# Optimization experiments

Measured on AMD Instinct MI355X. Metric: run time of the kernel, lower is better.

## Reference

```python
import jax, jax.numpy as jnp
import numpy as np

B, L, C = 8, 4096, 256  # batches, points per batch, channels
C8 = C // 8             # query/key projection dim


def setup_inputs() -> dict:
    key = jax.random.key(0)
    ks = jax.random.split(key, 8)
    feats = jax.random.normal(ks[0], (B * L, C), dtype=jnp.float32)
    s_in = 1.0 / np.sqrt(C)
    Wq = jax.random.normal(ks[1], (C8, C), dtype=jnp.float32) * s_in
    bq = jax.random.normal(ks[2], (C8,), dtype=jnp.float32) * 0.01
    Wk = jax.random.normal(ks[3], (C8, C), dtype=jnp.float32) * s_in
    bk = jax.random.normal(ks[4], (C8,), dtype=jnp.float32) * 0.01
    Wv = jax.random.normal(ks[5], (C, C), dtype=jnp.float32) * s_in
    bv = jax.random.normal(ks[6], (C,), dtype=jnp.float32) * 0.01
    # torch init is gamma=0 which zeroes the attention branch; use a nonzero
    # scalar so the attention path contributes to output/gradients.
    gamma = jnp.float32(0.5)
    return {"feats": feats, "Wq": Wq, "bq": bq, "Wk": Wk, "bk": bk,
            "Wv": Wv, "bv": bv, "gamma": gamma,
            "batch_size": B, "points_per_batch": L}


def reference(feats, Wq, bq, Wk, bk, Wv, bv, gamma, batch_size, points_per_batch):
    n, c = feats.shape
    x = feats.reshape(batch_size, points_per_batch, c)  # [B, L, C]
    # conv1d with kernel_size=1 == per-point linear projection
    q = jnp.einsum('blc,dc->bld', x, Wq) + bq  # [B, L, C8]
    k = jnp.einsum('blc,dc->bld', x, Wk) + bk  # [B, L, C8]
    v = jnp.einsum('blc,dc->bld', x, Wv) + bv  # [B, L, C]
    energy = jnp.einsum('bid,bjd->bij', q, k)  # unscaled scores [B, L, L]
    attn = jax.nn.softmax(energy, axis=-1)
    # torch: out[c, l] = sum_j V[c, j] * attn[l, j]  -> [B, C, L]
    out_cl = jnp.einsum('bjc,blj->bcl', v, attn)
    # faithful to torch .view(batch_size, C): raw reshape of [C, L] -> [L, C]
    out = out_cl.reshape(batch_size, points_per_batch, c)
    y = gamma * out + x
    return y.reshape(n, c)
```

## Files before the change

### kernel.cpp

```cpp
#include <hip/hip_runtime.h>

#define LOG2E 1.44269504088896340736f

typedef __attribute__((ext_vector_type(4))) float  f32x4;
typedef __attribute__((ext_vector_type(8))) __bf16 bf16x8;
typedef __attribute__((ext_vector_type(4))) __bf16 bf16x4;

static __device__ __forceinline__ f32x4 mfma16(bf16x8 a, bf16x8 b, f32x4 c) {
  return __builtin_amdgcn_mfma_f32_16x16x32_bf16(a, b, c, 0, 0, 0);
}


__global__ void cvt_f32_to_bf16(const float* __restrict__ s, __bf16* __restrict__ d, int n4) {
  const int stride = gridDim.x * blockDim.x;
  for (int i = blockIdx.x * blockDim.x + threadIdx.x; i < n4; i += stride) {
    const float4 v = reinterpret_cast<const float4*>(s)[i];
    bf16x4 o = { (__bf16)v.x, (__bf16)v.y, (__bf16)v.z, (__bf16)v.w };
    reinterpret_cast<bf16x4*>(d)[i] = o;
  }
}

__global__ __launch_bounds__(256) void cvt_weights(
    const float* __restrict__ wq, const float* __restrict__ wk, const float* __restrict__ wv,
    __bf16* __restrict__ dq, __bf16* __restrict__ dk, __bf16* __restrict__ dv) {
  const int i = blockIdx.x * 256 + threadIdx.x;
  const float* s; __bf16* d; int off;
  if (i < 2048)      { s = wq; d = dq; off = i; }
  else if (i < 4096) { s = wk; d = dk; off = i - 2048; }
  else               { s = wv; d = dv; off = i - 4096; }
  const float4 v = reinterpret_cast<const float4*>(s)[off];
  bf16x4 o = { (__bf16)v.x, (__bf16)v.y, (__bf16)v.z, (__bf16)v.w };
  reinterpret_cast<bf16x4*>(d)[off] = o;
}

__global__ __launch_bounds__(256) void qk_proj(
    const __bf16* __restrict__ x, const __bf16* __restrict__ wq, const __bf16* __restrict__ wk,
    const float* __restrict__ bq, const float* __restrict__ bk,
    __bf16* __restrict__ Qh, __bf16* __restrict__ Ql,
    __bf16* __restrict__ Kh, __bf16* __restrict__ Kl)
{
  const int w = threadIdx.x >> 6, lane = threadIdx.x & 63;
  const int lo = lane & 15, hi = lane >> 4;
  const int m0 = blockIdx.x * 64 + w * 16;
  f32x4 acc[4] = {};
  for (int ks = 0; ks < 8; ++ks) {
    const bf16x8 a = *reinterpret_cast<const bf16x8*>(x + (size_t)(m0 + lo) * 256 + ks * 32 + hi * 8);
    #pragma unroll
    for (int nt = 0; nt < 4; ++nt) {
      const int d = nt * 16 + lo;
      const __bf16* wrow = (nt < 2) ? (wq + d * 256) : (wk + (d - 32) * 256);
      const bf16x8 bfr = *reinterpret_cast<const bf16x8*>(wrow + ks * 32 + hi * 8);
      acc[nt] = mfma16(a, bfr, acc[nt]);
    }
  }
  #pragma unroll
  for (int nt = 0; nt < 4; ++nt) {
    const int d = nt * 16 + lo;
    const float bias = (nt < 2) ? bq[d] : bk[d - 32];
    #pragma unroll
    for (int r = 0; r < 4; ++r) {
      const size_t row = m0 + hi * 4 + r;
      float v = acc[nt][r] + bias;
      if (nt < 2) v *= LOG2E;
      const __bf16 vh = (__bf16)v;
      const __bf16 vl = (__bf16)(v - (float)vh);
      if (nt < 2) { Qh[row * 32 + d] = vh;        Ql[row * 32 + d] = vl; }
      else        { Kh[row * 32 + (d - 32)] = vh; Kl[row * 32 + (d - 32)] = vl; }
    }
  }
}

__global__ __launch_bounds__(256) void v_proj(
    const __bf16* __restrict__ x, const __bf16* __restrict__ wv, const float* __restrict__ bv,
    __bf16* __restrict__ VT)
{
  const int w = threadIdx.x >> 6, lane = threadIdx.x & 63;
  const int lo = lane & 15, hi = lane >> 4;
  const int bn = blockIdx.x & 511, bc = blockIdx.x >> 9;
  const int n0 = bn * 64;
  const int c0 = bc * 64 + w * 16;
  f32x4 acc[4] = {};
  for (int ks = 0; ks < 8; ++ks) {
    const bf16x8 a = *reinterpret_cast<const bf16x8*>(wv + (size_t)(c0 + lo) * 256 + ks * 32 + hi * 8);
    #pragma unroll
    for (int nt = 0; nt < 4; ++nt) {
      const bf16x8 bfr = *reinterpret_cast<const bf16x8*>(x + (size_t)(n0 + nt * 16 + lo) * 256 + ks * 32 + hi * 8);
      acc[nt] = mfma16(a, bfr, acc[nt]);
    }
  }
  const int bb = n0 >> 12;
  #pragma unroll
  for (int nt = 0; nt < 4; ++nt) {
    const int nl = n0 + nt * 16 + lo;
    #pragma unroll
    for (int r = 0; r < 4; ++r) {
      const int c = c0 + hi * 4 + r;
      VT[(size_t)(bb * 256 + c) * 4096 + (nl & 4095)] = (__bf16)(acc[nt][r] + bv[c]);
    }
  }
}

__global__ __launch_bounds__(256, 2) void attn_kernel(
    const __bf16* __restrict__ Qhi, const __bf16* __restrict__ Qlo,
    const __bf16* __restrict__ Khi, const __bf16* __restrict__ Klo,
    const __bf16* __restrict__ VT,
    const float* __restrict__ feats, const float* __restrict__ gptr,
    float* __restrict__ out)
{
  __shared__ alignas(16) __bf16 vlds[2][256 * 64];
  __shared__ alignas(16) __bf16 pbuf[4][16 * 64];

  const int tid  = threadIdx.x;
  const int w    = tid >> 6, lane = tid & 63;
  const int lo   = lane & 15, hi = lane >> 4;
  const int b    = blockIdx.x & 7;
  const int qt   = blockIdx.x >> 3;
  const int qblk = qt * 64;
  const int qw   = qblk + w * 16;

  const size_t qrow = (size_t)(b * 4096 + qw + lo) * 32 + hi * 8;
  const bf16x8 qh = *reinterpret_cast<const bf16x8*>(Qhi + qrow);
  const bf16x8 ql = *reinterpret_cast<const bf16x8*>(Qlo + qrow);

  const size_t kbase = (size_t)(b * 4096 + lo) * 32 + hi * 8;

  const int lsw = (lane & 7) ^ (lane >> 3);
  const __bf16* vstage_src0 = VT + (size_t)(b * 256 + w * 64 + (lane >> 3)) * 4096 + lsw * 8;

  char* const pw_base = (char*)&pbuf[w][0];
  const int swz = (lo & 7) << 4;

  f32x4 o[16] = {};
  f32x4 lacc4 = {0.f, 0.f, 0.f, 0.f};

  #define STAGE_V(JB, BUF)                                                        \
    {                                                                             \
      _Pragma("unroll")                                                           \
      for (int g = 0; g < 8; ++g) {                                               \
        __builtin_amdgcn_global_load_lds(                                         \
            (const __attribute__((address_space(1))) void*)(vstage_src0 + (size_t)g * 8 * 4096 + (JB)), \
            (__attribute__((address_space(3))) void*)(&vlds[BUF][(w * 64 + g * 8) * 64 + lane * 8]), \
            16, 0, 0);                                                            \
      }                                                                           \
    }

  STAGE_V(0, 0);
  bf16x8 kh[4], kl[4];
  #pragma unroll
  for (int jt = 0; jt < 4; ++jt) {
    kh[jt] = *reinterpret_cast<const bf16x8*>(Khi + kbase + (size_t)(jt * 16) * 32);
    kl[jt] = *reinterpret_cast<const bf16x8*>(Klo + kbase + (size_t)(jt * 16) * 32);
  }
  asm volatile("s_waitcnt vmcnt(0)" ::: "memory");
  __builtin_amdgcn_s_barrier();

  #pragma unroll 2
  for (int t = 0; t < 64; ++t) {
    const int jb  = t * 64;
    const int jn  = (jb + 64) & 4095;
    const int cur = t & 1, nxt = cur ^ 1;

    f32x4 s[4];
    #pragma unroll
    for (int jt = 0; jt < 4; ++jt) {
      f32x4 acc = {0.f, 0.f, 0.f, 0.f};
      acc = mfma16(kh[jt], qh, acc);
      acc = mfma16(kl[jt], qh, acc);
      acc = mfma16(kh[jt], ql, acc);
      s[jt] = acc;
    }

    STAGE_V(jn, nxt);
    asm volatile("" ::: "memory");
    __builtin_amdgcn_sched_barrier(0);

    bf16x8 kh2[4], kl2[4];
    #pragma unroll
    for (int jt = 0; jt < 4; ++jt) {
      kh2[jt] = *reinterpret_cast<const bf16x8*>(Khi + kbase + (size_t)(jn + jt * 16) * 32);
      kl2[jt] = *reinterpret_cast<const bf16x8*>(Klo + kbase + (size_t)(jn + jt * 16) * 32);
    }

    #pragma unroll
    for (int jt = 0; jt < 4; ++jt) {
      f32x4 p4;
      #pragma unroll
      for (int r = 0; r < 4; ++r) p4[r] = __builtin_amdgcn_exp2f(s[jt][r]);
      lacc4 += p4;
      bf16x4 pk = { (__bf16)p4[0], (__bf16)p4[1], (__bf16)p4[2], (__bf16)p4[3] };
      *reinterpret_cast<bf16x4*>(pw_base + lo * 128 + ((jt * 32 + hi * 8) ^ swz)) = pk;
    }

    bf16x8 pf[2];
    #pragma unroll
    for (int cc = 0; cc < 2; ++cc)
      pf[cc] = *reinterpret_cast<const bf16x8*>(pw_base + lo * 128 + ((cc * 64 + hi * 16) ^ swz));

    const __bf16* const vb_base = &vlds[cur][0];
    __builtin_amdgcn_s_setprio(1);
    #pragma unroll
    for (int cc = 0; cc < 2; ++cc) {
      #pragma unroll
      for (int ct = 0; ct < 16; ++ct) {
        const int c = ct * 16 + lo;
        const bf16x8 vb = *reinterpret_cast<const bf16x8*>(
            vb_base + c * 64 + ((((cc * 4 + hi) ^ (c & 7))) << 3));
        o[ct] = mfma16(pf[cc], vb, o[ct]);
      }
    }
    __builtin_amdgcn_s_setprio(0);

    asm volatile("s_waitcnt vmcnt(8) lgkmcnt(0)" ::: "memory");
    __builtin_amdgcn_sched_barrier(0);
    __builtin_amdgcn_s_barrier();
    asm volatile("" ::: "memory");
    __builtin_amdgcn_sched_barrier(0);

    #pragma unroll
    for (int jt = 0; jt < 4; ++jt) { kh[jt] = kh2[jt]; kl[jt] = kl2[jt]; }
  }
  #undef STAGE_V

  float lacc = lacc4[0] + lacc4[1] + lacc4[2] + lacc4[3];
  lacc += __shfl_xor(lacc, 16);
  lacc += __shfl_xor(lacc, 32);
  const float g = gptr[0];
  float inv[4];
  #pragma unroll
  for (int r = 0; r < 4; ++r) inv[r] = g / __shfl(lacc, hi * 4 + r);

  const size_t obase = (size_t)b * (256 * 4096);
  const int q_lo = qw + hi * 4;
  #pragma unroll
  for (int ct = 0; ct < 16; ++ct) {
    const int c = ct * 16 + lo;
    const size_t idx = obase + (size_t)c * 4096 + q_lo;
    const float4 xr = *reinterpret_cast<const float4*>(feats + idx);
    float4 y;
    y.x = o[ct][0] * inv[0] + xr.x;
    y.y = o[ct][1] * inv[1] + xr.y;
    y.z = o[ct][2] * inv[2] + xr.z;
    y.w = o[ct][3] * inv[3] + xr.w;
    *reinterpret_cast<float4*>(out + idx) = y;
  }
}

extern "C" void kernel_launch(void* const* d_in, const int* in_sizes, int n_in,
                              void* d_out, int out_size, void* d_ws, size_t ws_size,
                              hipStream_t stream) {
  const float* feats = (const float*)d_in[0];
  const float* Wq    = (const float*)d_in[1];
  const float* bq    = (const float*)d_in[2];
  const float* Wk    = (const float*)d_in[3];
  const float* bk    = (const float*)d_in[4];
  const float* Wv    = (const float*)d_in[5];
  const float* bv    = (const float*)d_in[6];
  const float* gamma = (const float*)d_in[7];
  float* out = (float*)d_out;

  char* ws = (char*)d_ws;
  const size_t SZ_X  = 16777216;
  const size_t SZ_QK = 2097152;
  const size_t SZ_VT = 16777216;
  const size_t NEED = SZ_X + 4 * SZ_QK + SZ_VT + 2 * 16384 + 131072;
  if (ws_size < NEED) return;

  __bf16* xb  = (__bf16*)(ws);
  __bf16* Qh  = (__bf16*)(ws + SZ_X);
  __bf16* Ql  = (__bf16*)(ws + SZ_X + SZ_QK);
  __bf16* Kh  = (__bf16*)(ws + SZ_X + 2 * SZ_QK);
  __bf16* Kl  = (__bf16*)(ws + SZ_X + 3 * SZ_QK);
  __bf16* VT  = (__bf16*)(ws + SZ_X + 4 * SZ_QK);
  __bf16* wqb = (__bf16*)(ws + SZ_X + 4 * SZ_QK + SZ_VT);
  __bf16* wkb = wqb + 32 * 256;
  __bf16* wvb = wkb + 32 * 256;

  cvt_f32_to_bf16<<<2048, 256, 0, stream>>>(feats, xb, 8388608 / 4);
  cvt_weights<<<80, 256, 0, stream>>>(Wq, Wk, Wv, wqb, wkb, wvb);

  qk_proj<<<512, 256, 0, stream>>>(xb, wqb, wkb, bq, bk, Qh, Ql, Kh, Kl);
  v_proj <<<2048, 256, 0, stream>>>(xb, wvb, bv, VT);
  attn_kernel<<<512, 256, 0, stream>>>(Qh, Ql, Kh, Kl, VT, feats, gamma, out);
}
```

Before: 190.5 us.

## Split attention key range across waves with 32x32 MFMA and LDS reduction

The attention kernel now gives each block 32 queries instead of 64 and splits each 64-key tile across the four waves. Each wave computes scores for its 16 keys, reads V fragments straight from global memory rather than staging them in LDS, and accumulates with 32x32x16 MFMAs. Partial outputs and row sums are then reduced across waves through LDS in a rotating exchange, and the grid doubles to 1024 blocks. The v_proj store is also changed to write packed bf16x4 vectors. This removes the per-iteration V staging and barrier, in exchange for more global V traffic (no reuse across waves) and a reduction epilogue that needs a large shared buffer.

```diff
diff --git a/kernel.cpp b/kernel.cpp
--- a/kernel.cpp
+++ b/kernel.cpp
@@ -2,12 +2,16 @@
 
 #define LOG2E 1.44269504088896340736f
 
-typedef __attribute__((ext_vector_type(4))) float  f32x4;
-typedef __attribute__((ext_vector_type(8))) __bf16 bf16x8;
-typedef __attribute__((ext_vector_type(4))) __bf16 bf16x4;
+typedef __attribute__((ext_vector_type(4)))  float  f32x4;
+typedef __attribute__((ext_vector_type(16))) float  f32x16;
+typedef __attribute__((ext_vector_type(8)))  __bf16 bf16x8;
+typedef __attribute__((ext_vector_type(4)))  __bf16 bf16x4;
 
 static __device__ __forceinline__ f32x4 mfma16(bf16x8 a, bf16x8 b, f32x4 c) {
   return __builtin_amdgcn_mfma_f32_16x16x32_bf16(a, b, c, 0, 0, 0);
+}
+static __device__ __forceinline__ f32x16 mfma32(bf16x8 a, bf16x8 b, f32x16 c) {
+  return __builtin_amdgcn_mfma_f32_32x32x16_bf16(a, b, c, 0, 0, 0);
 }
 
 
@@ -85,18 +89,18 @@
     #pragma unroll
     for (int nt = 0; nt < 4; ++nt) {
       const bf16x8 bfr = *reinterpret_cast<const bf16x8*>(x + (size_t)(n0 + nt * 16 + lo) * 256 + ks * 32 + hi * 8);
-      acc[nt] = mfma16(a, bfr, acc[nt]);
+      acc[nt] = mfma16(bfr, a, acc[nt]);
     }
   }
   const int bb = n0 >> 12;
+  const int c = c0 + lo;
+  const float bias = bv[c];
   #pragma unroll
   for (int nt = 0; nt < 4; ++nt) {
-    const int nl = n0 + nt * 16 + lo;
-    #pragma unroll
-    for (int r = 0; r < 4; ++r) {
-      const int c = c0 + hi * 4 + r;
-      VT[(size_t)(bb * 256 + c) * 4096 + (nl & 4095)] = (__bf16)(acc[nt][r] + bv[c]);
-    }
+    const int n = (n0 + nt * 16 + hi * 4) & 4095;
+    bf16x4 pk = { (__bf16)(acc[nt][0] + bias), (__bf16)(acc[nt][1] + bias),
+                  (__bf16)(acc[nt][2] + bias), (__bf16)(acc[nt][3] + bias) };
+    *reinterpret_cast<bf16x4*>(VT + (size_t)(bb * 256 + c) * 4096 + n) = pk;
   }
 }
 
@@ -107,142 +111,156 @@
     const float* __restrict__ feats, const float* __restrict__ gptr,
     float* __restrict__ out)
 {
-  __shared__ alignas(16) __bf16 vlds[2][256 * 64];
-  __shared__ alignas(16) __bf16 pbuf[4][16 * 64];
+  __shared__ alignas(16) __bf16 pt[4][32 * 24];
+  __shared__ alignas(16) float  ored[4][2048];
+  __shared__ float lred[4][32];
+  __shared__ float lsumbuf[32];
 
   const int tid  = threadIdx.x;
   const int w    = tid >> 6, lane = tid & 63;
   const int lo   = lane & 15, hi = lane >> 4;
+  const int l31  = lane & 31, h  = lane >> 5;
   const int b    = blockIdx.x & 7;
-  const int qt   = blockIdx.x >> 3;
-  const int qblk = qt * 64;
-  const int qw   = qblk + w * 16;
-
-  const size_t qrow = (size_t)(b * 4096 + qw + lo) * 32 + hi * 8;
-  const bf16x8 qh = *reinterpret_cast<const bf16x8*>(Qhi + qrow);
-  const bf16x8 ql = *reinterpret_cast<const bf16x8*>(Qlo + qrow);
-
-  const size_t kbase = (size_t)(b * 4096 + lo) * 32 + hi * 8;
-
-  const int lsw = (lane & 7) ^ (lane >> 3);
-  const __bf16* vstage_src0 = VT + (size_t)(b * 256 + w * 64 + (lane >> 3)) * 4096 + lsw * 8;
-
-  char* const pw_base = (char*)&pbuf[w][0];
-  const int swz = (lo & 7) << 4;
-
-  f32x4 o[16] = {};
-  f32x4 lacc4 = {0.f, 0.f, 0.f, 0.f};
-
-  #define STAGE_V(JB, BUF)                                                        \
-    {                                                                             \
-      _Pragma("unroll")                                                           \
-      for (int g = 0; g < 8; ++g) {                                               \
-        __builtin_amdgcn_global_load_lds(                                         \
-            (const __attribute__((address_space(1))) void*)(vstage_src0 + (size_t)g * 8 * 4096 + (JB)), \
-            (__attribute__((address_space(3))) void*)(&vlds[BUF][(w * 64 + g * 8) * 64 + lane * 8]), \
-            16, 0, 0);                                                            \
-      }                                                                           \
-    }
-
-  STAGE_V(0, 0);
-  bf16x8 kh[4], kl[4];
-  #pragma unroll
-  for (int jt = 0; jt < 4; ++jt) {
-    kh[jt] = *reinterpret_cast<const bf16x8*>(Khi + kbase + (size_t)(jt * 16) * 32);
-    kl[jt] = *reinterpret_cast<const bf16x8*>(Klo + kbase + (size_t)(jt * 16) * 32);
-  }
-  asm volatile("s_waitcnt vmcnt(0)" ::: "memory");
-  __builtin_amdgcn_s_barrier();
-
-  #pragma unroll 2
+  const int qb   = blockIdx.x >> 3;
+
+  bf16x8 qh[2], ql[2];
+  #pragma unroll
+  for (int qt = 0; qt < 2; ++qt) {
+    const int qi = (b * 4096 + qb * 32 + qt * 16 + lo) * 32 + hi * 8;
+    qh[qt] = *reinterpret_cast<const bf16x8*>(Qhi + qi);
+    ql[qt] = *reinterpret_cast<const bf16x8*>(Qlo + qi);
+  }
+
+  const int kidx = (b * 4096 + w * 16 + lo) * 32 + hi * 8;
+  int voff[8];
+  #pragma unroll
+  for (int ct = 0; ct < 8; ++ct)
+    voff[ct] = (b * 256 + ct * 32 + l31) * 4096 + w * 16 + h * 8;
+
+  char* const ptw = (char*)&pt[w][0];
+
+  f32x16 o[8] = {};
+  f32x4  lacc4[2] = {};
+
+  bf16x8 kh = *reinterpret_cast<const bf16x8*>(Khi + kidx);
+  bf16x8 kl = *reinterpret_cast<const bf16x8*>(Klo + kidx);
+
   for (int t = 0; t < 64; ++t) {
-    const int jb  = t * 64;
-    const int jn  = (jb + 64) & 4095;
-    const int cur = t & 1, nxt = cur ^ 1;
-
-    f32x4 s[4];
-    #pragma unroll
-    for (int jt = 0; jt < 4; ++jt) {
-      f32x4 acc = {0.f, 0.f, 0.f, 0.f};
-      acc = mfma16(kh[jt], qh, acc);
-      acc = mfma16(kl[jt], qh, acc);
-      acc = mfma16(kh[jt], ql, acc);
-      s[jt] = acc;
-    }
-
-    STAGE_V(jn, nxt);
-    asm volatile("" ::: "memory");
-    __builtin_amdgcn_sched_barrier(0);
-
-    bf16x8 kh2[4], kl2[4];
-    #pragma unroll
-    for (int jt = 0; jt < 4; ++jt) {
-      kh2[jt] = *reinterpret_cast<const bf16x8*>(Khi + kbase + (size_t)(jn + jt * 16) * 32);
-      kl2[jt] = *reinterpret_cast<const bf16x8*>(Klo + kbase + (size_t)(jn + jt * 16) * 32);
-    }
-
-    #pragma unroll
-    for (int jt = 0; jt < 4; ++jt) {
+    const int jb = t * 64;
+    const int jn = (jb + 64) & 4095;
+
+    bf16x8 vf[8];
+    #pragma unroll
+    for (int ct = 0; ct < 8; ++ct)
+      vf[ct] = *reinterpret_cast<const bf16x8*>(VT + voff[ct] + jb);
+
+    const bf16x8 kh2 = *reinterpret_cast<const bf16x8*>(Khi + kidx + jn * 32);
+    const bf16x8 kl2 = *reinterpret_cast<const bf16x8*>(Klo + kidx + jn * 32);
+
+    f32x4 s[2];
+    #pragma unroll
+    for (int qt = 0; qt < 2; ++qt) {
+      f32x4 a = {0.f, 0.f, 0.f, 0.f};
+      a = mfma16(kh, qh[qt], a);
+      a = mfma16(kl, qh[qt], a);
+      a = mfma16(kh, ql[qt], a);
+      s[qt] = a;
+    }
+
+    #pragma unroll
+    for (int qt = 0; qt < 2; ++qt) {
       f32x4 p4;
       #pragma unroll
-      for (int r = 0; r < 4; ++r) p4[r] = __builtin_amdgcn_exp2f(s[jt][r]);
-      lacc4 += p4;
+      for (int r = 0; r < 4; ++r) p4[r] = __builtin_amdgcn_exp2f(s[qt][r]);
+      lacc4[qt] += p4;
       bf16x4 pk = { (__bf16)p4[0], (__bf16)p4[1], (__bf16)p4[2], (__bf16)p4[3] };
-      *reinterpret_cast<bf16x4*>(pw_base + lo * 128 + ((jt * 32 + hi * 8) ^ swz)) = pk;
-    }
-
-    bf16x8 pf[2];
-    #pragma unroll
-    for (int cc = 0; cc < 2; ++cc)
-      pf[cc] = *reinterpret_cast<const bf16x8*>(pw_base + lo * 128 + ((cc * 64 + hi * 16) ^ swz));
-
-    const __bf16* const vb_base = &vlds[cur][0];
+      *reinterpret_cast<bf16x4*>(ptw + (qt * 16 + lo) * 48 + hi * 8) = pk;
+    }
+
+    const bf16x8 pa = *reinterpret_cast<const bf16x8*>(ptw + l31 * 48 + h * 16);
+
     __builtin_amdgcn_s_setprio(1);
     #pragma unroll
-    for (int cc = 0; cc < 2; ++cc) {
-      #pragma unroll
-      for (int ct = 0; ct < 16; ++ct) {
-        const int c = ct * 16 + lo;
-        const bf16x8 vb = *reinterpret_cast<const bf16x8*>(
-            vb_base + c * 64 + ((((cc * 4 + hi) ^ (c & 7))) << 3));
-        o[ct] = mfma16(pf[cc], vb, o[ct]);
-      }
-    }
+    for (int ct = 0; ct < 8; ++ct)
+      o[ct] = mfma32(pa, vf[ct], o[ct]);
     __builtin_amdgcn_s_setprio(0);
 
-    asm volatile("s_waitcnt vmcnt(8) lgkmcnt(0)" ::: "memory");
-    __builtin_amdgcn_sched_barrier(0);
-    __builtin_amdgcn_s_barrier();
-    asm volatile("" ::: "memory");
-    __builtin_amdgcn_sched_barrier(0);
-
-    #pragma unroll
-    for (int jt = 0; jt < 4; ++jt) { kh[jt] = kh2[jt]; kl[jt] = kl2[jt]; }
-  }
-  #undef STAGE_V
-
-  float lacc = lacc4[0] + lacc4[1] + lacc4[2] + lacc4[3];
-  lacc += __shfl_xor(lacc, 16);
-  lacc += __shfl_xor(lacc, 32);
+    kh = kh2; kl = kl2;
+  }
+
+  float la0 = lacc4[0][0] + lacc4[0][1] + lacc4[0][2] + lacc4[0][3];
+  float la1 = lacc4[1][0] + lacc4[1][1] + lacc4[1][2] + lacc4[1][3];
+  la0 += __shfl_xor(la0, 16); la0 += __shfl_xor(la0, 32);
+  la1 += __shfl_xor(la1, 16); la1 += __shfl_xor(la1, 32);
+  if (lane < 16) { lred[w][lane] = la0; lred[w][16 + lane] = la1; }
+  __syncthreads();
+  if (w == 0 && lane < 32)
+    lsumbuf[lane] = lred[0][lane] + lred[1][lane] + lred[2][lane] + lred[3][lane];
+  __syncthreads();
+
   const float g = gptr[0];
-  float inv[4];
-  #pragma unroll
-  for (int r = 0; r < 4; ++r) inv[r] = g / __shfl(lacc, hi * 4 + r);
-
-  const size_t obase = (size_t)b * (256 * 4096);
-  const int q_lo = qw + hi * 4;
-  #pragma unroll
-  for (int ct = 0; ct < 16; ++ct) {
-    const int c = ct * 16 + lo;
-    const size_t idx = obase + (size_t)c * 4096 + q_lo;
-    const float4 xr = *reinterpret_cast<const float4*>(feats + idx);
-    float4 y;
-    y.x = o[ct][0] * inv[0] + xr.x;
-    y.y = o[ct][1] * inv[1] + xr.y;
-    y.z = o[ct][2] * inv[2] + xr.z;
-    y.w = o[ct][3] * inv[3] + xr.w;
-    *reinterpret_cast<float4*>(out + idx) = y;
-  }
+  f32x4 inv4[4];
+  #pragma unroll
+  for (int k = 0; k < 4; ++k) {
+    const f32x4 lv = *reinterpret_cast<const f32x4*>(&lsumbuf[8 * k + 4 * h]);
+    inv4[k][0] = g / lv[0]; inv4[k][1] = g / lv[1];
+    inv4[k][2] = g / lv[2]; inv4[k][3] = g / lv[3];
+  }
+
+  #define OADDR(REG, CL, K) ((char*)&ored[REG][0] + (CL) * 128 + ((((2*(K)+h) ^ ((CL) & 7))) << 4))
+  #define SEND(M)                                                              \
+    { _Pragma("unroll") for (int ti = 0; ti < 2; ++ti) {                       \
+        const int cl = ti * 32 + l31;                                          \
+        _Pragma("unroll") for (int k = 0; k < 4; ++k) {                        \
+          f32x4 v = { o[2*(M)+ti][4*k], o[2*(M)+ti][4*k+1],                    \
+                      o[2*(M)+ti][4*k+2], o[2*(M)+ti][4*k+3] };                \
+          *reinterpret_cast<f32x4*>(OADDR(w, cl, k)) = v; } } }
+  #define RECV(M, SRC)                                                         \
+    { _Pragma("unroll") for (int ti = 0; ti < 2; ++ti) {                       \
+        const int cl = ti * 32 + l31;                                          \
+        _Pragma("unroll") for (int k = 0; k < 4; ++k) {                        \
+          const f32x4 v = *reinterpret_cast<const f32x4*>(OADDR(SRC, cl, k));  \
+          o[2*(M)+ti][4*k]   += v[0]; o[2*(M)+ti][4*k+1] += v[1];              \
+          o[2*(M)+ti][4*k+2] += v[2]; o[2*(M)+ti][4*k+3] += v[3]; } } }
+
+  #pragma unroll
+  for (int r = 1; r < 4; ++r) {
+    const int m = (w + r) & 3;
+    if      (m == 0) SEND(0)
+    else if (m == 1) SEND(1)
+    else if (m == 2) SEND(2)
+    else             SEND(3)
+    __syncthreads();
+    const int src = (w - r) & 3;
+    if      (w == 0) RECV(0, src)
+    else if (w == 1) RECV(1, src)
+    else if (w == 2) RECV(2, src)
+    else             RECV(3, src)
+    __syncthreads();
+  }
+  #undef OADDR
+  #undef SEND
+  #undef RECV
+
+  const int obase = b * (256 * 4096);
+  const int q0 = qb * 32 + 4 * h;
+  #define EPI(M)                                                               \
+    { _Pragma("unroll") for (int ti = 0; ti < 2; ++ti) {                       \
+        const int c = (2*(M)+ti) * 32 + l31;                                   \
+        _Pragma("unroll") for (int k = 0; k < 4; ++k) {                        \
+          const int idx = obase + c * 4096 + q0 + 8 * k;                       \
+          const float4 xr = *reinterpret_cast<const float4*>(feats + idx);     \
+          float4 y;                                                            \
+          y.x = o[2*(M)+ti][4*k]   * inv4[k][0] + xr.x;                        \
+          y.y = o[2*(M)+ti][4*k+1] * inv4[k][1] + xr.y;                        \
+          y.z = o[2*(M)+ti][4*k+2] * inv4[k][2] + xr.z;                        \
+          y.w = o[2*(M)+ti][4*k+3] * inv4[k][3] + xr.w;                        \
+          *reinterpret_cast<float4*>(out + idx) = y; } } }
+  if      (w == 0) EPI(0)
+  else if (w == 1) EPI(1)
+  else if (w == 2) EPI(2)
+  else             EPI(3)
+  #undef EPI
 }
 
 extern "C" void kernel_launch(void* const* d_in, const int* in_sizes, int n_in,
@@ -280,5 +298,5 @@
 
   qk_proj<<<512, 256, 0, stream>>>(xb, wqb, wkb, bq, bk, Qh, Ql, Kh, Kl);
   v_proj <<<2048, 256, 0, stream>>>(xb, wvb, bv, VT);
-  attn_kernel<<<512, 256, 0, stream>>>(Qh, Ql, Kh, Kl, VT, feats, gamma, out);
-}
+  attn_kernel<<<1024, 256, 0, stream>>>(Qh, Ql, Kh, Kl, VT, feats, gamma, out);
+}
```

After: 340.6 us. 78.8% more time.

## Switch PV product to 32x32x16 MFMA with 2x2 wave tiling

Applied to the files above, without the earlier changes.

Restructures the attention kernel so each wave owns 32 queries by 128 channels and computes P·V with 32x32x16 bf16 MFMAs instead of sixteen 16x16 tiles covering all 256 channels. This cuts the number of V LDS fragment reads per MFMA FLOP. V staging and the P buffer get new XOR swizzles, and row-sum normalization goes through LDS. The v_proj kernel also swaps MFMA operands so it writes packed bf16x4 vectors along the point dimension instead of scalar stores. The trade-off is that QK scores are now computed twice (each wave pair duplicates them for the same queries), and more layout complexity carries a risk of bank conflicts.

```diff
diff --git a/kernel.cpp b/kernel.cpp
--- a/kernel.cpp
+++ b/kernel.cpp
@@ -2,12 +2,16 @@
 
 #define LOG2E 1.44269504088896340736f
 
-typedef __attribute__((ext_vector_type(4))) float  f32x4;
-typedef __attribute__((ext_vector_type(8))) __bf16 bf16x8;
-typedef __attribute__((ext_vector_type(4))) __bf16 bf16x4;
+typedef __attribute__((ext_vector_type(4)))  float  f32x4;
+typedef __attribute__((ext_vector_type(16))) float  f32x16;
+typedef __attribute__((ext_vector_type(8)))  __bf16 bf16x8;
+typedef __attribute__((ext_vector_type(4)))  __bf16 bf16x4;
 
 static __device__ __forceinline__ f32x4 mfma16(bf16x8 a, bf16x8 b, f32x4 c) {
   return __builtin_amdgcn_mfma_f32_16x16x32_bf16(a, b, c, 0, 0, 0);
+}
+static __device__ __forceinline__ f32x16 mfma32(bf16x8 a, bf16x8 b, f32x16 c) {
+  return __builtin_amdgcn_mfma_f32_32x32x16_bf16(a, b, c, 0, 0, 0);
 }
 
 
@@ -85,18 +89,18 @@
     #pragma unroll
     for (int nt = 0; nt < 4; ++nt) {
       const bf16x8 bfr = *reinterpret_cast<const bf16x8*>(x + (size_t)(n0 + nt * 16 + lo) * 256 + ks * 32 + hi * 8);
-      acc[nt] = mfma16(a, bfr, acc[nt]);
+      acc[nt] = mfma16(bfr, a, acc[nt]);
     }
   }
   const int bb = n0 >> 12;
+  const int c = c0 + lo;
+  const float bias = bv[c];
   #pragma unroll
   for (int nt = 0; nt < 4; ++nt) {
-    const int nl = n0 + nt * 16 + lo;
-    #pragma unroll
-    for (int r = 0; r < 4; ++r) {
-      const int c = c0 + hi * 4 + r;
-      VT[(size_t)(bb * 256 + c) * 4096 + (nl & 4095)] = (__bf16)(acc[nt][r] + bv[c]);
-    }
+    const int n = (n0 + nt * 16 + hi * 4) & 4095;
+    bf16x4 pk = { (__bf16)(acc[nt][0] + bias), (__bf16)(acc[nt][1] + bias),
+                  (__bf16)(acc[nt][2] + bias), (__bf16)(acc[nt][3] + bias) };
+    *reinterpret_cast<bf16x4*>(VT + (size_t)(bb * 256 + c) * 4096 + n) = pk;
   }
 }
 
@@ -107,49 +111,69 @@
     const float* __restrict__ feats, const float* __restrict__ gptr,
     float* __restrict__ out)
 {
-  __shared__ alignas(16) __bf16 vlds[2][256 * 64];
-  __shared__ alignas(16) __bf16 pbuf[4][16 * 64];
+  __shared__ alignas(16) __bf16 vlds[2][16384];
+  __shared__ alignas(16) __bf16 pbuf[4][2048];
 
   const int tid  = threadIdx.x;
   const int w    = tid >> 6, lane = tid & 63;
   const int lo   = lane & 15, hi = lane >> 4;
+  const int l31  = lane & 31, h  = lane >> 5;
+  const int qg   = w & 1,    cg  = w >> 1;
   const int b    = blockIdx.x & 7;
-  const int qt   = blockIdx.x >> 3;
-  const int qblk = qt * 64;
-  const int qw   = qblk + w * 16;
-
-  const size_t qrow = (size_t)(b * 4096 + qw + lo) * 32 + hi * 8;
-  const bf16x8 qh = *reinterpret_cast<const bf16x8*>(Qhi + qrow);
-  const bf16x8 ql = *reinterpret_cast<const bf16x8*>(Qlo + qrow);
-
-  const size_t kbase = (size_t)(b * 4096 + lo) * 32 + hi * 8;
-
-  const int lsw = (lane & 7) ^ (lane >> 3);
-  const __bf16* vstage_src0 = VT + (size_t)(b * 256 + w * 64 + (lane >> 3)) * 4096 + lsw * 8;
-
-  char* const pw_base = (char*)&pbuf[w][0];
-  const int swz = (lo & 7) << 4;
-
-  f32x4 o[16] = {};
-  f32x4 lacc4 = {0.f, 0.f, 0.f, 0.f};
-
-  #define STAGE_V(JB, BUF)                                                        \
-    {                                                                             \
-      _Pragma("unroll")                                                           \
-      for (int g = 0; g < 8; ++g) {                                               \
-        __builtin_amdgcn_global_load_lds(                                         \
-            (const __attribute__((address_space(1))) void*)(vstage_src0 + (size_t)g * 8 * 4096 + (JB)), \
-            (__attribute__((address_space(3))) void*)(&vlds[BUF][(w * 64 + g * 8) * 64 + lane * 8]), \
-            16, 0, 0);                                                            \
-      }                                                                           \
+  const int qblk = (blockIdx.x >> 3) * 64;
+  const int qw   = qblk + qg * 32;
+
+  bf16x8 qh[2], ql[2];
+  #pragma unroll
+  for (int qt = 0; qt < 2; ++qt) {
+    const int qi = (b * 4096 + qw + qt * 16 + lo) * 32 + hi * 8;
+    qh[qt] = *reinterpret_cast<const bf16x8*>(Qhi + qi);
+    ql[qt] = *reinterpret_cast<const bf16x8*>(Qlo + qi);
+  }
+
+  const int kbase = (b * 4096 + lo) * 32 + hi * 8;
+
+  const int cc   = tid >> 3;
+  const int scc  = (tid & 7) ^ ((cc ^ (cc >> 3)) & 7);
+  const __bf16* const vsrc = VT + (size_t)(b * 256 + cc) * 4096;
+
+  int vrow[4], vsw[4];
+  #pragma unroll
+  for (int ct = 0; ct < 4; ++ct) {
+    const int row = cg * 128 + ct * 32 + l31;
+    vrow[ct] = row * 128;
+    vsw[ct]  = (row ^ (row >> 3)) & 7;
+  }
+  int swzq[2];
+  #pragma unroll
+  for (int qt = 0; qt < 2; ++qt) {
+    const int q = qt * 16 + lo;
+    swzq[qt] = (q ^ (q >> 3)) & 7;
+  }
+  const int swzp = (l31 ^ (l31 >> 3)) & 7;
+  char* const pwb = (char*)&pbuf[w][0];
+
+  f32x16 o[4] = {};
+  f32x4  lacc[2] = {};
+
+  #define STAGE_V(JB, BUF)                                                      \
+    {                                                                           \
+      _Pragma("unroll")                                                         \
+      for (int g = 0; g < 8; ++g) {                                             \
+        const int slot = scc ^ ((g & 1) << 2);                                  \
+        __builtin_amdgcn_global_load_lds(                                       \
+            (const __attribute__((address_space(1))) void*)(vsrc + (size_t)g * 32 * 4096 + (JB) + slot * 8), \
+            (__attribute__((address_space(3))) void*)(&vlds[BUF][g * 2048 + tid * 8]), \
+            16, 0, 0);                                                          \
+      }                                                                         \
     }
 
   STAGE_V(0, 0);
   bf16x8 kh[4], kl[4];
   #pragma unroll
   for (int jt = 0; jt < 4; ++jt) {
-    kh[jt] = *reinterpret_cast<const bf16x8*>(Khi + kbase + (size_t)(jt * 16) * 32);
-    kl[jt] = *reinterpret_cast<const bf16x8*>(Klo + kbase + (size_t)(jt * 16) * 32);
+    kh[jt] = *reinterpret_cast<const bf16x8*>(Khi + kbase + (jt * 16) * 32);
+    kl[jt] = *reinterpret_cast<const bf16x8*>(Klo + kbase + (jt * 16) * 32);
   }
   asm volatile("s_waitcnt vmcnt(0)" ::: "memory");
   __builtin_amdgcn_s_barrier();
@@ -160,14 +184,36 @@
     const int jn  = (jb + 64) & 4095;
     const int cur = t & 1, nxt = cur ^ 1;
 
-    f32x4 s[4];
-    #pragma unroll
-    for (int jt = 0; jt < 4; ++jt) {
-      f32x4 acc = {0.f, 0.f, 0.f, 0.f};
-      acc = mfma16(kh[jt], qh, acc);
-      acc = mfma16(kl[jt], qh, acc);
-      acc = mfma16(kh[jt], ql, acc);
-      s[jt] = acc;
+    #pragma unroll
+    for (int jp = 0; jp < 2; ++jp) {
+      f32x4 s[2][2];
+      #pragma unroll
+      for (int jj = 0; jj < 2; ++jj) {
+        const int jt = jp * 2 + jj;
+        #pragma unroll
+        for (int qt = 0; qt < 2; ++qt) {
+          f32x4 a = {0.f, 0.f, 0.f, 0.f};
+          a = mfma16(kh[jt], qh[qt], a);
+          a = mfma16(kl[jt], qh[qt], a);
+          a = mfma16(kh[jt], ql[qt], a);
+          s[jj][qt] = a;
+        }
+      }
+      #pragma unroll
+      for (int jj = 0; jj < 2; ++jj) {
+        const int jt = jp * 2 + jj;
+        #pragma unroll
+        for (int qt = 0; qt < 2; ++qt) {
+          f32x4 p4;
+          #pragma unroll
+          for (int r = 0; r < 4; ++r) p4[r] = __builtin_amdgcn_exp2f(s[jj][qt][r]);
+          lacc[qt] += p4;
+          bf16x4 pk = { (__bf16)p4[0], (__bf16)p4[1], (__bf16)p4[2], (__bf16)p4[3] };
+          const int q = qt * 16 + lo;
+          *reinterpret_cast<bf16x4*>(pwb + q * 128 +
+              (((jt * 2 + (hi >> 1)) ^ swzq[qt]) << 4) + ((hi & 1) << 3)) = pk;
+        }
+      }
     }
 
     STAGE_V(jn, nxt);
@@ -177,35 +223,24 @@
     bf16x8 kh2[4], kl2[4];
     #pragma unroll
     for (int jt = 0; jt < 4; ++jt) {
-      kh2[jt] = *reinterpret_cast<const bf16x8*>(Khi + kbase + (size_t)(jn + jt * 16) * 32);
-      kl2[jt] = *reinterpret_cast<const bf16x8*>(Klo + kbase + (size_t)(jn + jt * 16) * 32);
-    }
-
-    #pragma unroll
-    for (int jt = 0; jt < 4; ++jt) {
-      f32x4 p4;
+      kh2[jt] = *reinterpret_cast<const bf16x8*>(Khi + kbase + (jn + jt * 16) * 32);
+      kl2[jt] = *reinterpret_cast<const bf16x8*>(Klo + kbase + (jn + jt * 16) * 32);
+    }
+
+    bf16x8 pa[4];
+    #pragma unroll
+    for (int ks = 0; ks < 4; ++ks)
+      pa[ks] = *reinterpret_cast<const bf16x8*>(pwb + l31 * 128 + (((ks * 2 + h) ^ swzp) << 4));
+
+    const char* const vb = (const char*)&vlds[cur][0];
+    __builtin_amdgcn_s_setprio(1);
+    #pragma unroll
+    for (int ct = 0; ct < 4; ++ct) {
       #pragma unroll
-      for (int r = 0; r < 4; ++r) p4[r] = __builtin_amdgcn_exp2f(s[jt][r]);
-      lacc4 += p4;
-      bf16x4 pk = { (__bf16)p4[0], (__bf16)p4[1], (__bf16)p4[2], (__bf16)p4[3] };
-      *reinterpret_cast<bf16x4*>(pw_base + lo * 128 + ((jt * 32 + hi * 8) ^ swz)) = pk;
-    }
-
-    bf16x8 pf[2];
-    #pragma unroll
-    for (int cc = 0; cc < 2; ++cc)
-      pf[cc] = *reinterpret_cast<const bf16x8*>(pw_base + lo * 128 + ((cc * 64 + hi * 16) ^ swz));
-
-    const __bf16* const vb_base = &vlds[cur][0];
-    __builtin_amdgcn_s_setprio(1);
-    #pragma unroll
-    for (int cc = 0; cc < 2; ++cc) {
-      #pragma unroll
-      for (int ct = 0; ct < 16; ++ct) {
-        const int c = ct * 16 + lo;
-        const bf16x8 vb = *reinterpret_cast<const bf16x8*>(
-            vb_base + c * 64 + ((((cc * 4 + hi) ^ (c & 7))) << 3));
-        o[ct] = mfma16(pf[cc], vb, o[ct]);
+      for (int ks = 0; ks < 4; ++ks) {
+        const bf16x8 vf = *reinterpret_cast<const bf16x8*>(
+            vb + vrow[ct] + (((ks * 2 + h) ^ vsw[ct]) << 4));
+        o[ct] = mfma32(pa[ks], vf, o[ct]);
       }
     }
     __builtin_amdgcn_s_setprio(0);
@@ -221,27 +256,39 @@
   }
   #undef STAGE_V
 
-  float lacc = lacc4[0] + lacc4[1] + lacc4[2] + lacc4[3];
-  lacc += __shfl_xor(lacc, 16);
-  lacc += __shfl_xor(lacc, 32);
+  float la0 = lacc[0][0] + lacc[0][1] + lacc[0][2] + lacc[0][3];
+  float la1 = lacc[1][0] + lacc[1][1] + lacc[1][2] + lacc[1][3];
+  la0 += __shfl_xor(la0, 16); la0 += __shfl_xor(la0, 32);
+  la1 += __shfl_xor(la1, 16); la1 += __shfl_xor(la1, 32);
+  asm volatile("s_waitcnt lgkmcnt(0)" ::: "memory");
+  float* const lredw = (float*)&pbuf[w][0];
+  if (lane < 16) { lredw[lane] = la0; lredw[16 + lane] = la1; }
+
   const float g = gptr[0];
-  float inv[4];
-  #pragma unroll
-  for (int r = 0; r < 4; ++r) inv[r] = g / __shfl(lacc, hi * 4 + r);
-
-  const size_t obase = (size_t)b * (256 * 4096);
-  const int q_lo = qw + hi * 4;
-  #pragma unroll
-  for (int ct = 0; ct < 16; ++ct) {
-    const int c = ct * 16 + lo;
-    const size_t idx = obase + (size_t)c * 4096 + q_lo;
-    const float4 xr = *reinterpret_cast<const float4*>(feats + idx);
-    float4 y;
-    y.x = o[ct][0] * inv[0] + xr.x;
-    y.y = o[ct][1] * inv[1] + xr.y;
-    y.z = o[ct][2] * inv[2] + xr.z;
-    y.w = o[ct][3] * inv[3] + xr.w;
-    *reinterpret_cast<float4*>(out + idx) = y;
+  f32x4 inv[4];
+  #pragma unroll
+  for (int a = 0; a < 4; ++a) {
+    const f32x4 lv = *reinterpret_cast<const f32x4*>(&lredw[8 * a + 4 * h]);
+    inv[a][0] = g / lv[0]; inv[a][1] = g / lv[1];
+    inv[a][2] = g / lv[2]; inv[a][3] = g / lv[3];
+  }
+
+  const int obase = b * (256 * 4096);
+  const int q0 = qblk + qg * 32 + 4 * h;
+  #pragma unroll
+  for (int ct = 0; ct < 4; ++ct) {
+    const int c = cg * 128 + ct * 32 + l31;
+    #pragma unroll
+    for (int a = 0; a < 4; ++a) {
+      const int idx = obase + c * 4096 + q0 + 8 * a;
+      const float4 xr = *reinterpret_cast<const float4*>(feats + idx);
+      float4 y;
+      y.x = o[ct][4 * a]     * inv[a][0] + xr.x;
+      y.y = o[ct][4 * a + 1] * inv[a][1] + xr.y;
+      y.z = o[ct][4 * a + 2] * inv[a][2] + xr.z;
+      y.w = o[ct][4 * a + 3] * inv[a][3] + xr.w;
+      *reinterpret_cast<float4*>(out + idx) = y;
+    }
   }
 }
 
```

Measured after the change: 212.5 us. +11.6%, slower.

## Restructure attention to 8-wave blocks with 32x32 MFMA PV and software-pipelined P

Applied to the files above, without the earlier changes.

The attention kernel moves to 512-thread blocks. Work is split into 4 query tiles by 2 key halves for the score stage, and each wave owns 32 channels for the PV stage using 32x32x16 MFMAs on a shared P buffer. The P·V product for the previous tile is overlapped with loading and scoring the next tile through double-buffered P and V in LDS, and row sums are combined across waves through LDS at the end. The V projection is also changed to write packed bf16x4 transposed stores instead of scalar ones. The aims are better MFMA efficiency and fewer, wider stores, at the cost of more LDS traffic, a block-wide barrier every iteration and higher occupancy demands.

```diff
diff --git a/kernel.cpp b/kernel.cpp
--- a/kernel.cpp
+++ b/kernel.cpp
@@ -2,12 +2,16 @@
 
 #define LOG2E 1.44269504088896340736f
 
-typedef __attribute__((ext_vector_type(4))) float  f32x4;
-typedef __attribute__((ext_vector_type(8))) __bf16 bf16x8;
-typedef __attribute__((ext_vector_type(4))) __bf16 bf16x4;
+typedef __attribute__((ext_vector_type(4)))  float  f32x4;
+typedef __attribute__((ext_vector_type(16))) float  f32x16;
+typedef __attribute__((ext_vector_type(8)))  __bf16 bf16x8;
+typedef __attribute__((ext_vector_type(4)))  __bf16 bf16x4;
 
 static __device__ __forceinline__ f32x4 mfma16(bf16x8 a, bf16x8 b, f32x4 c) {
   return __builtin_amdgcn_mfma_f32_16x16x32_bf16(a, b, c, 0, 0, 0);
+}
+static __device__ __forceinline__ f32x16 mfma32(bf16x8 a, bf16x8 b, f32x16 c) {
+  return __builtin_amdgcn_mfma_f32_32x32x16_bf16(a, b, c, 0, 0, 0);
 }
 
 
@@ -85,163 +89,202 @@
     #pragma unroll
     for (int nt = 0; nt < 4; ++nt) {
       const bf16x8 bfr = *reinterpret_cast<const bf16x8*>(x + (size_t)(n0 + nt * 16 + lo) * 256 + ks * 32 + hi * 8);
-      acc[nt] = mfma16(a, bfr, acc[nt]);
+      acc[nt] = mfma16(bfr, a, acc[nt]);
     }
   }
   const int bb = n0 >> 12;
+  const int c = c0 + lo;
+  const float bias = bv[c];
   #pragma unroll
   for (int nt = 0; nt < 4; ++nt) {
-    const int nl = n0 + nt * 16 + lo;
-    #pragma unroll
-    for (int r = 0; r < 4; ++r) {
-      const int c = c0 + hi * 4 + r;
-      VT[(size_t)(bb * 256 + c) * 4096 + (nl & 4095)] = (__bf16)(acc[nt][r] + bv[c]);
-    }
-  }
-}
-
-__global__ __launch_bounds__(256, 2) void attn_kernel(
+    const int n = (n0 + nt * 16 + hi * 4) & 4095;
+    bf16x4 pk = { (__bf16)(acc[nt][0] + bias), (__bf16)(acc[nt][1] + bias),
+                  (__bf16)(acc[nt][2] + bias), (__bf16)(acc[nt][3] + bias) };
+    *reinterpret_cast<bf16x4*>(VT + (size_t)(bb * 256 + c) * 4096 + n) = pk;
+  }
+}
+
+__global__ __launch_bounds__(512, 4) void attn_kernel(
     const __bf16* __restrict__ Qhi, const __bf16* __restrict__ Qlo,
     const __bf16* __restrict__ Khi, const __bf16* __restrict__ Klo,
     const __bf16* __restrict__ VT,
     const float* __restrict__ feats, const float* __restrict__ gptr,
     float* __restrict__ out)
 {
-  __shared__ alignas(16) __bf16 vlds[2][256 * 64];
-  __shared__ alignas(16) __bf16 pbuf[4][16 * 64];
-
-  const int tid  = threadIdx.x;
-  const int w    = tid >> 6, lane = tid & 63;
-  const int lo   = lane & 15, hi = lane >> 4;
+  __shared__ alignas(16) __bf16 vlds[2][8][2048];
+  __shared__ alignas(16) __bf16 pbuf[2][4096];
+
+  const int tid = threadIdx.x;
+  const int w   = tid >> 6, lane = tid & 63;
+  const int lo  = lane & 15, hi = lane >> 4;
+  const int l31 = lane & 31, h  = lane >> 5;
+  const int qt  = w & 3, jtp = w >> 2;
   const int b    = blockIdx.x & 7;
-  const int qt   = blockIdx.x >> 3;
-  const int qblk = qt * 64;
-  const int qw   = qblk + w * 16;
-
-  const size_t qrow = (size_t)(b * 4096 + qw + lo) * 32 + hi * 8;
-  const bf16x8 qh = *reinterpret_cast<const bf16x8*>(Qhi + qrow);
-  const bf16x8 ql = *reinterpret_cast<const bf16x8*>(Qlo + qrow);
-
-  const size_t kbase = (size_t)(b * 4096 + lo) * 32 + hi * 8;
-
-  const int lsw = (lane & 7) ^ (lane >> 3);
-  const __bf16* vstage_src0 = VT + (size_t)(b * 256 + w * 64 + (lane >> 3)) * 4096 + lsw * 8;
-
-  char* const pw_base = (char*)&pbuf[w][0];
-  const int swz = (lo & 7) << 4;
-
-  f32x4 o[16] = {};
-  f32x4 lacc4 = {0.f, 0.f, 0.f, 0.f};
+  const int qblk = (blockIdx.x >> 3) * 64;
+
+  const int qi = (b * 4096 + qblk + qt * 16 + lo) * 32 + hi * 8;
+  const bf16x8 qh = *reinterpret_cast<const bf16x8*>(Qhi + qi);
+  const bf16x8 ql = *reinterpret_cast<const bf16x8*>(Qlo + qi);
+
+  const int kbase = (b * 4096 + jtp * 32 + lo) * 32 + hi * 8;
+
+  const int r_l = lane >> 3, s_l = lane & 7;
+  const __bf16* vsrc[4];
+  #pragma unroll
+  for (int g = 0; g < 4; ++g) {
+    const int row = w * 32 + g * 8 + r_l;
+    const int sw  = s_l ^ ((r_l ^ g) & 7);
+    vsrc[g] = VT + (size_t)(b * 256 + row) * 4096 + sw * 8;
+  }
+
+  const int q   = qt * 16 + lo;
+  const int swq = (q ^ (q >> 3)) & 7;
+  int swp[2], prow[2];
+  #pragma unroll
+  for (int qg = 0; qg < 2; ++qg) {
+    const int qq = qg * 32 + l31;
+    prow[qg] = qq * 128;
+    swp[qg]  = (qq ^ (qq >> 3)) & 7;
+  }
+  const int vrow = l31 * 128;
+  const int swv  = (l31 ^ (l31 >> 3)) & 7;
+
+  f32x16 o0 = {}, o1 = {};
+  f32x4  lacc = {};
 
   #define STAGE_V(JB, BUF)                                                        \
-    {                                                                             \
+    { _Pragma("unroll")                                                           \
+      for (int g = 0; g < 4; ++g) {                                               \
+        __builtin_amdgcn_global_load_lds(                                         \
+            (const __attribute__((address_space(1))) void*)(vsrc[g] + (JB)),      \
+            (__attribute__((address_space(3))) void*)(&vlds[BUF][w][g * 512 + lane * 8]), \
+            16, 0, 0);                                                            \
+      } }
+
+  #define PV_STEP(PRV)                                                            \
+    { const char* const pr = (const char*)&pbuf[PRV][0];                          \
+      const char* const vr = (const char*)&vlds[PRV][w][0] + vrow;                \
+      bf16x8 pa0[4], pa1[4], vf[4];                                               \
       _Pragma("unroll")                                                           \
-      for (int g = 0; g < 8; ++g) {                                               \
-        __builtin_amdgcn_global_load_lds(                                         \
-            (const __attribute__((address_space(1))) void*)(vstage_src0 + (size_t)g * 8 * 4096 + (JB)), \
-            (__attribute__((address_space(3))) void*)(&vlds[BUF][(w * 64 + g * 8) * 64 + lane * 8]), \
-            16, 0, 0);                                                            \
+      for (int ks = 0; ks < 4; ++ks) {                                            \
+        pa0[ks] = *reinterpret_cast<const bf16x8*>(pr + prow[0] + ((((ks * 2 + h) ^ swp[0])) << 4)); \
+        pa1[ks] = *reinterpret_cast<const bf16x8*>(pr + prow[1] + ((((ks * 2 + h) ^ swp[1])) << 4)); \
+        vf[ks]  = *reinterpret_cast<const bf16x8*>(vr + ((((ks * 2 + h) ^ swv)) << 4)); \
       }                                                                           \
-    }
-
-  STAGE_V(0, 0);
-  bf16x8 kh[4], kl[4];
-  #pragma unroll
-  for (int jt = 0; jt < 4; ++jt) {
-    kh[jt] = *reinterpret_cast<const bf16x8*>(Khi + kbase + (size_t)(jt * 16) * 32);
-    kl[jt] = *reinterpret_cast<const bf16x8*>(Klo + kbase + (size_t)(jt * 16) * 32);
-  }
-  asm volatile("s_waitcnt vmcnt(0)" ::: "memory");
-  __builtin_amdgcn_s_barrier();
-
-  #pragma unroll 2
-  for (int t = 0; t < 64; ++t) {
-    const int jb  = t * 64;
-    const int jn  = (jb + 64) & 4095;
-    const int cur = t & 1, nxt = cur ^ 1;
-
-    f32x4 s[4];
-    #pragma unroll
-    for (int jt = 0; jt < 4; ++jt) {
-      f32x4 acc = {0.f, 0.f, 0.f, 0.f};
-      acc = mfma16(kh[jt], qh, acc);
-      acc = mfma16(kl[jt], qh, acc);
-      acc = mfma16(kh[jt], ql, acc);
-      s[jt] = acc;
-    }
-
-    STAGE_V(jn, nxt);
-    asm volatile("" ::: "memory");
-    __builtin_amdgcn_sched_barrier(0);
-
-    bf16x8 kh2[4], kl2[4];
-    #pragma unroll
-    for (int jt = 0; jt < 4; ++jt) {
-      kh2[jt] = *reinterpret_cast<const bf16x8*>(Khi + kbase + (size_t)(jn + jt * 16) * 32);
-      kl2[jt] = *reinterpret_cast<const bf16x8*>(Klo + kbase + (size_t)(jn + jt * 16) * 32);
-    }
-
-    #pragma unroll
-    for (int jt = 0; jt < 4; ++jt) {
+      __builtin_amdgcn_s_setprio(1);                                              \
+      _Pragma("unroll")                                                           \
+      for (int ks = 0; ks < 4; ++ks) {                                            \
+        o0 = mfma32(pa0[ks], vf[ks], o0);                                         \
+        o1 = mfma32(pa1[ks], vf[ks], o1);                                         \
+      }                                                                           \
+      __builtin_amdgcn_s_setprio(0); }
+
+  {
+    const bf16x8 kh0 = *reinterpret_cast<const bf16x8*>(Khi + kbase);
+    const bf16x8 kl0 = *reinterpret_cast<const bf16x8*>(Klo + kbase);
+    const bf16x8 kh1 = *reinterpret_cast<const bf16x8*>(Khi + kbase + 512);
+    const bf16x8 kl1 = *reinterpret_cast<const bf16x8*>(Klo + kbase + 512);
+    STAGE_V(0, 0);
+    __builtin_amdgcn_sched_barrier(0);
+    #pragma unroll
+    for (int jj = 0; jj < 2; ++jj) {
+      const bf16x8 kh_ = jj ? kh1 : kh0;
+      const bf16x8 kl_ = jj ? kl1 : kl0;
+      f32x4 s_ = {0.f, 0.f, 0.f, 0.f};
+      s_ = mfma16(kh_, qh, s_);
+      s_ = mfma16(kl_, qh, s_);
+      s_ = mfma16(kh_, ql, s_);
       f32x4 p4;
       #pragma unroll
-      for (int r = 0; r < 4; ++r) p4[r] = __builtin_amdgcn_exp2f(s[jt][r]);
-      lacc4 += p4;
+      for (int r = 0; r < 4; ++r) p4[r] = __builtin_amdgcn_exp2f(s_[r]);
+      lacc += p4;
       bf16x4 pk = { (__bf16)p4[0], (__bf16)p4[1], (__bf16)p4[2], (__bf16)p4[3] };
-      *reinterpret_cast<bf16x4*>(pw_base + lo * 128 + ((jt * 32 + hi * 8) ^ swz)) = pk;
-    }
-
-    bf16x8 pf[2];
-    #pragma unroll
-    for (int cc = 0; cc < 2; ++cc)
-      pf[cc] = *reinterpret_cast<const bf16x8*>(pw_base + lo * 128 + ((cc * 64 + hi * 16) ^ swz));
-
-    const __bf16* const vb_base = &vlds[cur][0];
-    __builtin_amdgcn_s_setprio(1);
-    #pragma unroll
-    for (int cc = 0; cc < 2; ++cc) {
+      const int slot = ((jtp * 2 + jj) * 2 + (hi >> 1)) ^ swq;
+      *reinterpret_cast<bf16x4*>((char*)&pbuf[0][0] + q * 128 + (slot << 4) + ((hi & 1) << 3)) = pk;
+    }
+    asm volatile("s_waitcnt lgkmcnt(0)" ::: "memory");
+    __builtin_amdgcn_sched_barrier(0);
+    __builtin_amdgcn_s_barrier();
+  }
+
+  #pragma unroll 2
+  for (int t = 1; t < 64; ++t) {
+    const int jb  = t * 64;
+    const int cur = t & 1, prv = cur ^ 1;
+
+    asm volatile("s_waitcnt vmcnt(0)" ::: "memory");
+    __builtin_amdgcn_sched_barrier(0);
+
+    const bf16x8 kh0 = *reinterpret_cast<const bf16x8*>(Khi + kbase + jb * 32);
+    const bf16x8 kl0 = *reinterpret_cast<const bf16x8*>(Klo + kbase + jb * 32);
+    const bf16x8 kh1 = *reinterpret_cast<const bf16x8*>(Khi + kbase + jb * 32 + 512);
+    const bf16x8 kl1 = *reinterpret_cast<const bf16x8*>(Klo + kbase + jb * 32 + 512);
+    STAGE_V(jb, cur);
+    __builtin_amdgcn_sched_barrier(0);
+
+    PV_STEP(prv);
+
+    asm volatile("s_waitcnt vmcnt(4)" ::: "memory");
+    __builtin_amdgcn_sched_barrier(0);
+
+    #pragma unroll
+    for (int jj = 0; jj < 2; ++jj) {
+      const bf16x8 kh_ = jj ? kh1 : kh0;
+      const bf16x8 kl_ = jj ? kl1 : kl0;
+      f32x4 s_ = {0.f, 0.f, 0.f, 0.f};
+      s_ = mfma16(kh_, qh, s_);
+      s_ = mfma16(kl_, qh, s_);
+      s_ = mfma16(kh_, ql, s_);
+      f32x4 p4;
       #pragma unroll
-      for (int ct = 0; ct < 16; ++ct) {
-        const int c = ct * 16 + lo;
-        const bf16x8 vb = *reinterpret_cast<const bf16x8*>(
-            vb_base + c * 64 + ((((cc * 4 + hi) ^ (c & 7))) << 3));
-        o[ct] = mfma16(pf[cc], vb, o[ct]);
-      }
-    }
-    __builtin_amdgcn_s_setprio(0);
-
-    asm volatile("s_waitcnt vmcnt(8) lgkmcnt(0)" ::: "memory");
+      for (int r = 0; r < 4; ++r) p4[r] = __builtin_amdgcn_exp2f(s_[r]);
+      lacc += p4;
+      bf16x4 pk = { (__bf16)p4[0], (__bf16)p4[1], (__bf16)p4[2], (__bf16)p4[3] };
+      const int slot = ((jtp * 2 + jj) * 2 + (hi >> 1)) ^ swq;
+      *reinterpret_cast<bf16x4*>((char*)&pbuf[cur][0] + q * 128 + (slot << 4) + ((hi & 1) << 3)) = pk;
+    }
+
+    asm volatile("s_waitcnt lgkmcnt(0)" ::: "memory");
     __builtin_amdgcn_sched_barrier(0);
     __builtin_amdgcn_s_barrier();
     asm volatile("" ::: "memory");
-    __builtin_amdgcn_sched_barrier(0);
-
-    #pragma unroll
-    for (int jt = 0; jt < 4; ++jt) { kh[jt] = kh2[jt]; kl[jt] = kl2[jt]; }
-  }
+  }
+
+  asm volatile("s_waitcnt vmcnt(0)" ::: "memory");
+  __builtin_amdgcn_sched_barrier(0);
+  PV_STEP(1);
+
   #undef STAGE_V
-
-  float lacc = lacc4[0] + lacc4[1] + lacc4[2] + lacc4[3];
-  lacc += __shfl_xor(lacc, 16);
-  lacc += __shfl_xor(lacc, 32);
+  #undef PV_STEP
+
+  float la = lacc[0] + lacc[1] + lacc[2] + lacc[3];
+  la += __shfl_xor(la, 16);
+  la += __shfl_xor(la, 32);
+  float* const lp = (float*)&pbuf[0][0];
+  __syncthreads();
+  if (lane < 16) lp[jtp * 64 + qt * 16 + lo] = la;
+  __syncthreads();
+
   const float g = gptr[0];
-  float inv[4];
-  #pragma unroll
-  for (int r = 0; r < 4; ++r) inv[r] = g / __shfl(lacc, hi * 4 + r);
-
-  const size_t obase = (size_t)b * (256 * 4096);
-  const int q_lo = qw + hi * 4;
-  #pragma unroll
-  for (int ct = 0; ct < 16; ++ct) {
-    const int c = ct * 16 + lo;
-    const size_t idx = obase + (size_t)c * 4096 + q_lo;
-    const float4 xr = *reinterpret_cast<const float4*>(feats + idx);
-    float4 y;
-    y.x = o[ct][0] * inv[0] + xr.x;
-    y.y = o[ct][1] * inv[1] + xr.y;
-    y.z = o[ct][2] * inv[2] + xr.z;
-    y.w = o[ct][3] * inv[3] + xr.w;
-    *reinterpret_cast<float4*>(out + idx) = y;
+  const int c = w * 32 + l31;
+  const size_t obase = (size_t)b * (256 * 4096) + (size_t)c * 4096 + qblk;
+  #pragma unroll
+  for (int qg = 0; qg < 2; ++qg) {
+    const f32x16& o_ = qg ? o1 : o0;
+    #pragma unroll
+    for (int grp = 0; grp < 4; ++grp) {
+      const int q0 = qg * 32 + grp * 8 + 4 * h;
+      const f32x4 lv0 = *reinterpret_cast<const f32x4*>(&lp[q0]);
+      const f32x4 lv1 = *reinterpret_cast<const f32x4*>(&lp[64 + q0]);
+      const size_t idx = obase + q0;
+      const float4 xr = *reinterpret_cast<const float4*>(feats + idx);
+      float4 y;
+      y.x = o_[grp * 4 + 0] * (g / (lv0[0] + lv1[0])) + xr.x;
+      y.y = o_[grp * 4 + 1] * (g / (lv0[1] + lv1[1])) + xr.y;
+      y.z = o_[grp * 4 + 2] * (g / (lv0[2] + lv1[2])) + xr.z;
+      y.w = o_[grp * 4 + 3] * (g / (lv0[3] + lv1[3])) + xr.w;
+      *reinterpret_cast<float4*>(out + idx) = y;
+    }
   }
 }
 
@@ -280,5 +323,5 @@
 
   qk_proj<<<512, 256, 0, stream>>>(xb, wqb, wkb, bq, bk, Qh, Ql, Kh, Kl);
   v_proj <<<2048, 256, 0, stream>>>(xb, wvb, bv, VT);
-  attn_kernel<<<512, 256, 0, stream>>>(Qh, Ql, Kh, Kl, VT, feats, gamma, out);
-}
+  attn_kernel<<<512, 512, 0, stream>>>(Qh, Ql, Kh, Kl, VT, feats, gamma, out);
+}
```

After: 309.1 us. +62.3%, slower.
